# Kernel tuning notes

Measured on AMD Instinct MI355X. Metric: run time of the kernel, lower is better.

## Reference

```python
import jax, jax.numpy as jnp
import numpy as np

NQ = 4096
N0, N1 = 32768, 8192
N = N0 + N1
F = 128          # emb_dim (32x0e+32x1e)
H = 4            # num_heads
HD = F // H
NB = 64          # fc_neurons[0] radial basis size
DEG = 32
CUTOFFS = jnp.array([2.0, 4.0], dtype=jnp.float32)
OFFSETS = jnp.array([0.1, 0.2], dtype=jnp.float32)


def _sph_harm(u):
    # component-normalized real spherical harmonics l=0,1,2 of unit vectors u [E,3]
    x, y, z = u[:, 0], u[:, 1], u[:, 2]
    s3, s15, s5 = 3.0 ** 0.5, 15.0 ** 0.5, 5.0 ** 0.5
    return jnp.stack([
        jnp.ones_like(x),
        s3 * x, s3 * y, s3 * z,
        s15 * x * y, s15 * y * z, 0.5 * s5 * (3.0 * z * z - 1.0),
        s15 * x * z, 0.5 * s15 * (x * x - y * y),
    ], axis=-1)  # [E,9]


def setup_inputs() -> dict:
    key = jax.random.key(0)
    ks = jax.random.split(key, 20)
    E0 = NQ * DEG
    E1 = NQ * DEG
    edge_src = jnp.concatenate([
        jax.random.randint(ks[0], (E0,), 0, N0),
        jax.random.randint(ks[1], (E1,), N0, N),
    ])
    edge_dst = jnp.concatenate([
        jax.random.randint(ks[2], (E0,), 0, NQ),
        jax.random.randint(ks[3], (E1,), 0, NQ),
    ])
    scale_id = jnp.concatenate([jnp.zeros((E0,), jnp.int32), jnp.ones((E1,), jnp.int32)])
    r = lambda k, sh, s=1.0: jax.random.normal(k, sh, jnp.float32) * s
    return {
        'query_coord': r(ks[4], (NQ, 3)),
        'node_feature': r(ks[5], (N, F)),
        'node_coord': r(ks[6], (N, 3)),
        'edge_src': edge_src, 'edge_dst': edge_dst, 'scale_id': scale_id,
        'b_dst': r(ks[7], (F,)),
        'Wq': r(ks[8], (F, F), F ** -0.5),
        'Wk': r(ks[9], (F, F), F ** -0.5),
        'Wv': r(ks[10], (F, F), F ** -0.5),
        'Wo': r(ks[11], (F, F), F ** -0.5),
        'bo': r(ks[12], (F,)),
        'W_rad0': r(ks[13], (NB, NB), NB ** -0.5), 'b_rad0': r(ks[14], (NB,)),
        'W_rad1': r(ks[15], (NB, NB), NB ** -0.5), 'b_rad1': r(ks[16], (NB,)),
        'W_msg': r(ks[17], (NB, F), NB ** -0.5),
        'W_sh': r(ks[18], (9, F), 9 ** -0.5),
        'W_alpha': r(ks[19], (NB, H), NB ** -0.5),
    }


def _forward(query_coord, node_feature, node_coord, b_dst, Wq, Wk, Wv, Wo, bo,
             W_rad0, b_rad0, W_rad1, b_rad1, W_msg, W_sh, W_alpha,
             edge_src, edge_dst, scale_id):
    Nq = query_coord.shape[0]
    vec = node_coord[edge_src] - query_coord[edge_dst]            # [E,3]
    rlen = jnp.sqrt(jnp.sum(vec * vec, -1) + 1e-12)               # [E]
    off = OFFSETS[scale_id]
    cut = CUTOFFS[scale_id]
    xn = (rlen - off) / (cut - off)                               # normalized radius per scale
    centers = jnp.linspace(0.0, 1.0, NB)
    std = 1.0 / NB
    g = jnp.exp(-0.5 * ((xn[:, None] - centers) / std) ** 2)      # [E,NB] gaussian RBF
    soft = 0.5 * (1.0 + jnp.cos(jnp.pi * jnp.clip((xn - 0.8) / 0.2, 0.0, 1.0)))
    g = g * soft[:, None]                                         # soft finite cutoff
    # per-scale Linear after radial basis (2 scales, masked select)
    edge_scalar = jnp.where((scale_id == 0)[:, None], g @ W_rad0 + b_rad0, g @ W_rad1 + b_rad1)
    sh = _sph_harm(vec / rlen[:, None])                           # [E,9]
    # attention GNN (equiformer-style): dst features start as zeros + learned bias
    q = (b_dst @ Wq).reshape(H, HD)
    k = (node_feature @ Wk)[edge_src].reshape(-1, H, HD)
    logits = jnp.einsum('hd,ehd->eh', q, k) / (HD ** 0.5) + edge_scalar @ W_alpha  # [E,H]
    m = jax.ops.segment_max(logits, edge_dst, num_segments=Nq)
    p = jnp.exp(logits - m[edge_dst])
    denom = jax.ops.segment_sum(p, edge_dst, num_segments=Nq)
    alpha = p / (denom[edge_dst] + 1e-9)                          # segment softmax [E,H]
    v_e = (node_feature @ Wv)[edge_src] * (edge_scalar @ W_msg) + sh @ W_sh  # [E,F]
    msg = (alpha[:, :, None] * v_e.reshape(-1, H, HD)).reshape(-1, F)
    out = jax.ops.segment_sum(msg, edge_dst, num_segments=Nq)     # [Nq,F]
    return out @ Wo + bo


def reference(query_coord, node_feature, node_coord, edge_src, edge_dst, scale_id,
              b_dst, Wq, Wk, Wv, Wo, bo, W_rad0, b_rad0, W_rad1, b_rad1,
              W_msg, W_sh, W_alpha):
    return _forward(query_coord, node_feature, node_coord, b_dst, Wq, Wk, Wv, Wo, bo,
                    W_rad0, b_rad0, W_rad1, b_rad1, W_msg, W_sh, W_alpha,
                    edge_src, edge_dst, scale_id)
```

## Files before the change

### kernel.cpp

```cpp
#include <hip/hip_runtime.h>
#include <hip/hip_bf16.h>
#include <math.h>

#define PI_F 3.14159265358979323846f

typedef __attribute__((ext_vector_type(8))) short short8v;
typedef __attribute__((ext_vector_type(4))) float f32x4;

__device__ __forceinline__ short f2bf(float x) {
    return __builtin_bit_cast(short, __float2bfloat16(x));
}
__device__ __forceinline__ float bf2f(unsigned short u) {
    return __uint_as_float(((unsigned)u) << 16);
}
__device__ __forceinline__ int pack_bf2(float a, float b) {
    return (int)(unsigned short)f2bf(a) | ((int)(unsigned short)f2bf(b) << 16);
}

static const size_t WS_WA     = 0;
static const size_t WS_BA     = 512;
static const size_t WS_BM     = 520;
static const size_t WS_WMF    = 776;
static const size_t WS_WSHF   = 8968;
static const size_t WS_QKF    = 11016;
static const size_t WS_WVF    = 12040;
static const size_t WS_WOF    = 20232;
static const size_t WS_COUNTS = 28424;
static const size_t WS_OFFS   = 36624;
static const size_t WS_CURSOR = 44824;
static const size_t WS_PACKED = 53016;
static const size_t WS_LK     = 315160;
static const size_t WS_EDP    = 479000;
static const size_t WS_EDG    = 1527576;
static const size_t WS_VB     = 2576152;
static const size_t WS_OUTPRE = 5197592;

__global__ __launch_bounds__(256) void k_prepfmt(
    const float* b_dst, const float* Wq, const float* Wk,
    const float* W_rad0, const float* b_rad0,
    const float* W_rad1, const float* b_rad1,
    const float* W_msg, const float* W_alpha, const float* Wv,
    const float* Wo, const float* W_sh,
    float* Wa, float* ba, float* bm,
    short* WmF, short* WshF, short* QKF, short* WVF, short* WOF,
    int* counts, int nkey) {
    __shared__ float qs_s[128];
    __shared__ float qk_s[512];
    int t = threadIdx.x;
    int b = blockIdx.x;
    if (b == 0) {
        for (int i = t; i < nkey; i += 256) counts[i] = 0;
        if (t < 128) {
            float acc = 0.f;
            for (int c = 0; c < 128; ++c) acc += b_dst[c] * Wq[c * 128 + t];
            qs_s[t] = acc;
        }
        __syncthreads();
        if (t < 128) {
            const float invs = 0.17677669529663687f;
            for (int h = 0; h < 4; ++h) {
                float acc = 0.f;
                for (int d = 0; d < 32; ++d)
                    acc += Wk[t * 128 + h * 32 + d] * qs_s[h * 32 + d];
                qk_s[t * 4 + h] = acc * invs;
            }
        }
        for (int idx = t; idx < 512; idx += 256) {
            int s = idx >> 8, i = (idx >> 2) & 63, h = idx & 3;
            const float* Wr = s ? W_rad1 : W_rad0;
            float acc = 0.f;
            for (int u = 0; u < 64; ++u) acc += Wr[i * 64 + u] * W_alpha[u * 4 + h];
            Wa[idx] = acc;
        }
        if (t < 8) {
            int s = t >> 2, h = t & 3;
            const float* br = s ? b_rad1 : b_rad0;
            float acc = 0.f;
            for (int u = 0; u < 64; ++u) acc += br[u] * W_alpha[u * 4 + h];
            ba[t] = acc;
        }
        {
            int s = t >> 7, c = t & 127;
            const float* br = s ? b_rad1 : b_rad0;
            float acc = 0.f;
            for (int u = 0; u < 64; ++u) acc += br[u] * W_msg[u * 128 + c];
            bm[t] = acc;
        }
        __syncthreads();
        for (int idx = t; idx < 2048; idx += 256) {
            int j = idx & 7, lane = (idx >> 3) & 63, kh = idx >> 9;
            int k = kh * 32 + ((lane >> 4) << 3) + j;
            int col = lane & 15;
            QKF[idx] = f2bf(col < 4 ? qk_s[k * 4 + col] : 0.f);
        }
    } else {
        int item = (b - 1) * 256 + t;
        if (item < 16384) {
            int j = item & 7, lane = (item >> 3) & 63, kh = (item >> 9) & 1;
            int ct = (item >> 10) & 7, sid = item >> 13;
            int k = kh * 32 + ((lane >> 4) << 3) + j;
            int c = (lane & 15) * 8 + ct;
            const float* Wr = sid ? W_rad1 : W_rad0;
            float acc = 0.f;
            for (int u = 0; u < 64; ++u) acc += Wr[k * 64 + u] * W_msg[u * 128 + c];
            WmF[item] = f2bf(acc);
        } else if (item < 20480) {
            int i2 = item - 16384;
            int j = i2 & 7, lane = (i2 >> 3) & 63, ct = (i2 >> 9) & 7;
            int k = ((lane >> 4) << 3) + j;
            int c = (lane & 15) * 8 + ct;
            WshF[i2] = f2bf(k < 9 ? W_sh[k * 128 + c] : 0.f);
        } else if (item < 36864) {
            int i2 = item - 20480;
            int j = i2 & 7, lane = (i2 >> 3) & 63, ct = (i2 >> 9) & 7, kh = (i2 >> 12) & 3;
            int k = kh * 32 + ((lane >> 4) << 3) + j;
            int c = (lane & 15) * 8 + ct;
            WVF[i2] = f2bf(Wv[k * 128 + c]);
        } else {
            int i2 = item - 36864;
            int j = i2 & 7, lane = (i2 >> 3) & 63, ct = (i2 >> 9) & 7, kh = (i2 >> 12) & 3;
            int k = kh * 32 + ((lane >> 4) << 3) + j;
            int c = (lane & 15) * 8 + ct;
            WOF[i2] = f2bf(Wo[k * 128 + c]);
        }
    }
}

template <typename OUT, bool LK>
__global__ __launch_bounds__(256) void k_mgemm(
    const float* A, const short* WF, const float* bias, OUT* out,
    float* lk, const short* QKF, int M) {
    int t = threadIdx.x;
    int w = t >> 6, lane = t & 63;
    int m = lane & 15, grp = lane >> 4;
    int row0 = (blockIdx.x * 4 + w) * 16;
    if (row0 >= M) return;

    short8v a[4];
#pragma unroll
    for (int kh = 0; kh < 4; ++kh) {
        const float* ap = &A[(size_t)(row0 + m) * 128 + kh * 32 + grp * 8];
        float4 f0 = *(const float4*)ap;
        float4 f1 = *(const float4*)(ap + 4);
        a[kh][0] = f2bf(f0.x); a[kh][1] = f2bf(f0.y);
        a[kh][2] = f2bf(f0.z); a[kh][3] = f2bf(f0.w);
        a[kh][4] = f2bf(f1.x); a[kh][5] = f2bf(f1.y);
        a[kh][6] = f2bf(f1.z); a[kh][7] = f2bf(f1.w);
    }
    if constexpr (LK) {
        f32x4 cl = {0.f, 0.f, 0.f, 0.f};
#pragma unroll
        for (int kh = 0; kh < 4; ++kh) {
            short8v qb = *(const short8v*)&QKF[(kh * 64 + lane) * 8];
            cl = __builtin_amdgcn_mfma_f32_16x16x32_bf16(a[kh], qb, cl, 0, 0, 0);
        }
        if (m < 4) {
#pragma unroll
            for (int r = 0; r < 4; ++r)
                lk[(size_t)(row0 + grp * 4 + r) * 4 + m] = cl[r];
        }
    }
    f32x4 c8[8];
#pragma unroll
    for (int ct = 0; ct < 8; ++ct) {
        f32x4 c = {0.f, 0.f, 0.f, 0.f};
#pragma unroll
        for (int kh = 0; kh < 4; ++kh) {
            short8v bf = *(const short8v*)&WF[((kh * 8 + ct) * 64 + lane) * 8];
            c = __builtin_amdgcn_mfma_f32_16x16x32_bf16(a[kh], bf, c, 0, 0, 0);
        }
        c8[ct] = c;
    }
    if constexpr (sizeof(OUT) == 2) {
#pragma unroll
        for (int r = 0; r < 4; ++r) {
            int row = row0 + grp * 4 + r;
            int4 sv;
            sv.x = pack_bf2(c8[0][r], c8[1][r]);
            sv.y = pack_bf2(c8[2][r], c8[3][r]);
            sv.z = pack_bf2(c8[4][r], c8[5][r]);
            sv.w = pack_bf2(c8[6][r], c8[7][r]);
            *(int4*)&out[(size_t)row * 128 + m * 8] = sv;
        }
    } else {
        float4 b0 = make_float4(0.f, 0.f, 0.f, 0.f), b1 = b0;
        if (bias) {
            b0 = *(const float4*)&bias[m * 8];
            b1 = *(const float4*)&bias[m * 8 + 4];
        }
#pragma unroll
        for (int r = 0; r < 4; ++r) {
            int row = row0 + grp * 4 + r;
            float4 o0 = make_float4(c8[0][r] + b0.x, c8[1][r] + b0.y,
                                    c8[2][r] + b0.z, c8[3][r] + b0.w);
            float4 o1 = make_float4(c8[4][r] + b1.x, c8[5][r] + b1.y,
                                    c8[6][r] + b1.z, c8[7][r] + b1.w);
            *(float4*)&out[(size_t)row * 128 + m * 8] = o0;
            *(float4*)&out[(size_t)row * 128 + m * 8 + 4] = o1;
        }
    }
}

__global__ void k_hist(const int* edge_dst, const int* scale_id, int* counts, int E, int NQr) {
    int e = blockIdx.x * 256 + threadIdx.x;
    if (e < E) atomicAdd(&counts[scale_id[e] * NQr + edge_dst[e]], 1);
}

__global__ void k_scan(const int* counts, int* offsets, int* cursor, int nkey) {
    __shared__ int sdata[256];
    int t = threadIdx.x;
    int chunk = (nkey + 255) / 256;
    int sum = 0;
    for (int i = 0; i < chunk; ++i) {
        int idx = t * chunk + i;
        sum += (idx < nkey) ? counts[idx] : 0;
    }
    sdata[t] = sum;
    __syncthreads();
    for (int off = 1; off < 256; off <<= 1) {
        int v = (t >= off) ? sdata[t - off] : 0;
        __syncthreads();
        sdata[t] += v;
        __syncthreads();
    }
    int run = sdata[t] - sum;
    for (int i = 0; i < chunk; ++i) {
        int idx = t * chunk + i;
        if (idx < nkey) {
            offsets[idx] = run;
            cursor[idx] = run;
            run += counts[idx];
        }
    }
    if (t == 255) offsets[nkey] = sdata[255];
}

__global__ __launch_bounds__(256) void k_scatter_edge(
    const int* edge_src, const int* edge_dst, const int* scale_id,
    const float* qc, const float* nc, const float* lk,
    const float* WaB, const float* baB, int* cursor,
    int* packed, float* edP, float* edG, int E, int NQr) {
    __shared__ float WaS[512];
    __shared__ float baS[8];
    int t = threadIdx.x;
    for (int i = t; i < 512; i += 256) WaS[i] = WaB[i];
    if (t < 8) baS[t] = baB[t];
    __syncthreads();
    int e = blockIdx.x * 256 + t;
    if (e >= E) return;
    int src = edge_src[e], dst = edge_dst[e], sid = scale_id[e];
    int pos = atomicAdd(&cursor[sid * NQr + dst], 1);

    float qx = qc[dst * 3 + 0], qy = qc[dst * 3 + 1], qz = qc[dst * 3 + 2];
    float vx = nc[src * 3 + 0] - qx;
    float vy = nc[src * 3 + 1] - qy;
    float vz = nc[src * 3 + 2] - qz;
    float r = sqrtf(vx * vx + vy * vy + vz * vz + 1e-12f);
    float rinv = 1.0f / r;
    float ux = vx * rinv, uy = vy * rinv, uz = vz * rinv;

    float roff = sid ? 0.2f : 0.1f;
    float rdiv = sid ? (1.0f / 3.8f) : (1.0f / 1.9f);
    float xn = (r - roff) * rdiv;
    float su = fminf(fmaxf((xn - 0.8f) * 5.0f, 0.0f), 1.0f);
    float soft = 0.5f * (1.0f + __cosf(PI_F * su));

    float4 lkv = *(const float4*)&lk[(size_t)src * 4];

    const float qs = 64.f / 63.f;
    const float Qc = __expf(-qs * qs);
    const float* Wrow = WaS + sid * 256;
    float a0 = 0.f, a1 = 0.f, a2 = 0.f, a3 = 0.f;
#pragma unroll
    for (int ch = 0; ch < 8; ++ch) {
        float d = (xn - (float)(ch * 8) * (1.0f / 63.0f)) * 64.0f;
        float g = __expf(-0.5f * d * d);
        float tt = __expf(fminf(qs * d - 0.5f * qs * qs, 60.f));
#pragma unroll
        for (int j = 0; j < 8; ++j) {
            float4 wa = *(const float4*)&Wrow[(ch * 8 + j) * 4];
            a0 = fmaf(g, wa.x, a0);
            a1 = fmaf(g, wa.y, a1);
            a2 = fmaf(g, wa.z, a2);
            a3 = fmaf(g, wa.w, a3);
            g *= tt; tt *= Qc;
        }
    }
    float p0 = __expf(lkv.x + soft * a0 + baS[sid * 4 + 0]);
    float p1 = __expf(lkv.y + soft * a1 + baS[sid * 4 + 1]);
    float p2 = __expf(lkv.z + soft * a2 + baS[sid * 4 + 2]);
    float p3 = __expf(lkv.w + soft * a3 + baS[sid * 4 + 3]);
    packed[pos] = src | (dst << 16);
    *(float4*)&edP[(size_t)pos * 4] = make_float4(p0, p1, p2, p3);
    *(float4*)&edG[(size_t)pos * 4] = make_float4(ux, uy, uz, xn);
}

__device__ __forceinline__ short8v gchain(float xn, int k0, float soft, float Qc) {
    const float qs = 64.f / 63.f;
    float d = (xn - (float)k0 * (1.0f / 63.0f)) * 64.0f;
    float g = __expf(-0.5f * d * d);
    float tt = __expf(fminf(qs * d - 0.5f * qs * qs, 60.f));
    short8v rr;
#pragma unroll
    for (int j = 0; j < 8; ++j) {
        rr[j] = f2bf(g * soft);
        g *= tt; tt *= Qc;
    }
    return rr;
}

__global__ __launch_bounds__(256) void k_main6(
    const int* offsets, const int* packed, const float* edP, const float* edG,
    const unsigned short* Vu, const float* bm, const short* WmF, const short* WshF,
    float* out_pre, int NQr) {
    __shared__ float part[4][136];
    int t = threadIdx.x;
    int w = t >> 6, lane = t & 63;
    int dst = blockIdx.x;
    int sid = w & 1, par = w >> 1;
    int m = lane & 15, grp = lane >> 4;
    int h = m >> 2;

    float acc[8];
#pragma unroll
    for (int i = 0; i < 8; ++i) acc[i] = 0.f;
    float den = 0.f;

    int key = sid * NQr + dst;
    int s0 = offsets[key], s1 = offsets[key + 1];
    int n = s1 - s0;

    float4 bm0 = *(const float4*)&bm[sid * 128 + m * 8];
    float4 bm1 = *(const float4*)&bm[sid * 128 + m * 8 + 4];
    float bmv[8] = {bm0.x, bm0.y, bm0.z, bm0.w, bm1.x, bm1.y, bm1.z, bm1.w};

    const float qs = 64.f / 63.f;
    const float Qc = __expf(-qs * qs);
    const float s3 = 1.7320508075688772f, s15 = 3.872983346207417f, s5 = 2.23606797749979f;

    int ntiles = (n + 15) >> 4;
    if (n > 0 && par < ntiles) {
        auto load_tile = [&](int tl, float4& G4o, float (&pho)[4], int4 (&vvo)[4]) {
            int q0 = s0 + tl * 16;
            int posA = q0 + m; if (posA >= s1) posA = s1 - 1;
            G4o = *(const float4*)&edG[(size_t)posA * 4];
            int srcs[4];
#pragma unroll
            for (int r = 0; r < 4; ++r) {
                int pos = q0 + grp * 4 + r;
                bool valid = pos < s1;
                if (!valid) pos = s1 - 1;
                int wv = packed[pos];
                srcs[r] = wv & 0xFFFF;
                float4 pv = *(const float4*)&edP[(size_t)pos * 4];
                float p = (h & 2) ? ((h & 1) ? pv.w : pv.z)
                                  : ((h & 1) ? pv.y : pv.x);
                pho[r] = valid ? p : 0.f;
            }
#pragma unroll
            for (int r = 0; r < 4; ++r)
                vvo[r] = *(const int4*)&Vu[(size_t)srcs[r] * 128 + m * 8];
        };

        float4 G4c; float phc[4]; int4 vvc[4];
        load_tile(par, G4c, phc, vvc);

        for (int tl = par; tl < ntiles; tl += 2) {
            bool hasNext = (tl + 2) < ntiles;
            float4 G4n; float phn[4]; int4 vvn[4];
            if (hasNext) load_tile(tl + 2, G4n, phn, vvn);

            int wds[4][4] = {{vvc[0].x, vvc[0].y, vvc[0].z, vvc[0].w},
                             {vvc[1].x, vvc[1].y, vvc[1].z, vvc[1].w},
                             {vvc[2].x, vvc[2].y, vvc[2].z, vvc[2].w},
                             {vvc[3].x, vvc[3].y, vvc[3].z, vvc[3].w}};
            den += phc[0] + phc[1] + phc[2] + phc[3];

            float xn = G4c.w;
            float su = fminf(fmaxf((xn - 0.8f) * 5.0f, 0.0f), 1.0f);
            float soft = 0.5f * (1.0f + __cosf(PI_F * su));
            short8v aG0 = gchain(xn, grp * 8, soft, Qc);
            short8v aG1 = gchain(xn, 32 + grp * 8, soft, Qc);

            float ux = G4c.x, uy = G4c.y, uz = G4c.z;
            float sh[9];
            sh[0] = 1.f; sh[1] = s3 * ux; sh[2] = s3 * uy; sh[3] = s3 * uz;
            sh[4] = s15 * ux * uy; sh[5] = s15 * uy * uz;
            sh[6] = 0.5f * s5 * (3.f * uz * uz - 1.f);
            sh[7] = s15 * ux * uz; sh[8] = 0.5f * s15 * (ux * ux - uy * uy);
            short8v aS;
#pragma unroll
            for (int j = 0; j < 8; ++j) {
                float v = (grp == 0) ? sh[j] : ((grp == 1 && j == 0) ? sh[8] : 0.f);
                aS[j] = f2bf(v);
            }

#pragma unroll
            for (int ct = 0; ct < 8; ++ct) {
                short8v b0 = *(const short8v*)&WmF[(((sid * 8 + ct) * 2 + 0) * 64 + lane) * 8];
                short8v b1 = *(const short8v*)&WmF[(((sid * 8 + ct) * 2 + 1) * 64 + lane) * 8];
                short8v bS = *(const short8v*)&WshF[(ct * 64 + lane) * 8];
                f32x4 cms = {0.f, 0.f, 0.f, 0.f};
                cms = __builtin_amdgcn_mfma_f32_16x16x32_bf16(aG0, b0, cms, 0, 0, 0);
                cms = __builtin_amdgcn_mfma_f32_16x16x32_bf16(aG1, b1, cms, 0, 0, 0);
                f32x4 csh = {0.f, 0.f, 0.f, 0.f};
                csh = __builtin_amdgcn_mfma_f32_16x16x32_bf16(aS, bS, csh, 0, 0, 0);
#pragma unroll
                for (int r = 0; r < 4; ++r) {
                    int word = wds[r][ct >> 1];
                    unsigned short vu = (ct & 1) ? (unsigned short)(word >> 16)
                                                 : (unsigned short)(word & 0xFFFF);
                    float vf = bf2f(vu);
                    float ve = fmaf(vf, cms[r] + bmv[ct], csh[r]);
                    acc[ct] = fmaf(phc[r], ve, acc[ct]);
                }
            }

            if (hasNext) {
                G4c = G4n;
#pragma unroll
                for (int r = 0; r < 4; ++r) { phc[r] = phn[r]; vvc[r] = vvn[r]; }
            }
        }
    }

#pragma unroll
    for (int i = 0; i < 8; ++i) {
        acc[i] += __shfl_xor(acc[i], 16);
        acc[i] += __shfl_xor(acc[i], 32);
    }
    den += __shfl_xor(den, 16);
    den += __shfl_xor(den, 32);
    if (lane < 16) {
#pragma unroll
        for (int ct = 0; ct < 8; ++ct) part[w][lane * 8 + ct] = acc[ct];
        if ((lane & 3) == 0) part[w][128 + (lane >> 2)] = den;
    }
    __syncthreads();
    if (t < 128) {
        int hh = t >> 5;
        float s = part[0][t] + part[1][t] + part[2][t] + part[3][t];
        float d = part[0][128 + hh] + part[1][128 + hh] +
                  part[2][128 + hh] + part[3][128 + hh];
        out_pre[(size_t)dst * 128 + t] = s / (d + 1e-9f);
    }
}

extern "C" void kernel_launch(void* const* d_in, const int* in_sizes, int n_in,
                              void* d_out, int out_size, void* d_ws, size_t ws_size,
                              hipStream_t stream) {
    const float* query_coord = (const float*)d_in[0];
    const float* node_feature = (const float*)d_in[1];
    const float* node_coord = (const float*)d_in[2];
    const int* edge_src = (const int*)d_in[3];
    const int* edge_dst = (const int*)d_in[4];
    const int* scale_id = (const int*)d_in[5];
    const float* b_dst = (const float*)d_in[6];
    const float* Wq = (const float*)d_in[7];
    const float* Wk = (const float*)d_in[8];
    const float* Wv = (const float*)d_in[9];
    const float* Wo = (const float*)d_in[10];
    const float* bo = (const float*)d_in[11];
    const float* W_rad0 = (const float*)d_in[12];
    const float* b_rad0 = (const float*)d_in[13];
    const float* W_rad1 = (const float*)d_in[14];
    const float* b_rad1 = (const float*)d_in[15];
    const float* W_msg = (const float*)d_in[16];
    const float* W_sh = (const float*)d_in[17];
    const float* W_alpha = (const float*)d_in[18];
    (void)n_in; (void)ws_size; (void)out_size;

    int NQr = in_sizes[0] / 3;
    int Nn = in_sizes[1] / 128;
    int E = in_sizes[3];
    int nkey = NQr * 2;

    float* ws = (float*)d_ws;
    float* Wa = ws + WS_WA;
    float* ba = ws + WS_BA;
    float* bm = ws + WS_BM;
    short* WmF = (short*)(ws + WS_WMF);
    short* WshF = (short*)(ws + WS_WSHF);
    short* QKF = (short*)(ws + WS_QKF);
    short* WVF = (short*)(ws + WS_WVF);
    short* WOF = (short*)(ws + WS_WOF);
    int* counts = (int*)(ws + WS_COUNTS);
    int* offsets = (int*)(ws + WS_OFFS);
    int* cursor = (int*)(ws + WS_CURSOR);
    int* packed = (int*)(ws + WS_PACKED);
    float* lk = ws + WS_LK;
    float* edP = ws + WS_EDP;
    float* edG = ws + WS_EDG;
    unsigned short* Vb = (unsigned short*)(ws + WS_VB);
    float* out_pre = ws + WS_OUTPRE;
    float* out = (float*)d_out;

    hipLaunchKernelGGL(k_prepfmt, dim3(209), dim3(256), 0, stream,
                       b_dst, Wq, Wk, W_rad0, b_rad0, W_rad1, b_rad1, W_msg, W_alpha,
                       Wv, Wo, W_sh, Wa, ba, bm, WmF, WshF, QKF, WVF, WOF, counts, nkey);
    hipLaunchKernelGGL((k_mgemm<unsigned short, true>), dim3((Nn + 63) / 64), dim3(256), 0,
                       stream, node_feature, WVF, (const float*)nullptr, Vb, lk, QKF, Nn);
    hipLaunchKernelGGL(k_hist, dim3((E + 255) / 256), dim3(256), 0, stream,
                       edge_dst, scale_id, counts, E, NQr);
    hipLaunchKernelGGL(k_scan, dim3(1), dim3(256), 0, stream, counts, offsets, cursor, nkey);
    hipLaunchKernelGGL(k_scatter_edge, dim3((E + 255) / 256), dim3(256), 0, stream,
                       edge_src, edge_dst, scale_id, query_coord, node_coord, lk,
                       Wa, ba, cursor, packed, edP, edG, E, NQr);
    hipLaunchKernelGGL(k_main6, dim3(NQr), dim3(256), 0, stream,
                       offsets, packed, edP, edG, Vb, bm, WmF, WshF, out_pre, NQr);
    hipLaunchKernelGGL((k_mgemm<float, false>), dim3((NQr + 63) / 64), dim3(256), 0, stream,
                       out_pre, WOF, bo, out, (float*)nullptr, (const short*)nullptr, NQr);
}
```

Before: 153.1 us.

## Map one wave per destination in main kernel and fuse histogram into prep

The main aggregation kernel now gives each wavefront a whole destination, walking the tiles of both scales in sequence. Before, four waves per destination split the work by scale and parity and then combined partial sums through shared memory with a block barrier. The edge histogram moves into the prep kernel as extra blocks, and the counts are zeroed with a memset, which removes one launch. The trade-off is less parallelism per destination, so longer serial tile loops per wave and possible load imbalance when degrees vary.

New measurement: 147.0 us. 4.0% less time.

```diff
diff --git a/kernel.cpp b/kernel.cpp
--- a/kernel.cpp
+++ b/kernel.cpp
@@ -41,15 +41,15 @@
     const float* W_rad1, const float* b_rad1,
     const float* W_msg, const float* W_alpha, const float* Wv,
     const float* Wo, const float* W_sh,
+    const int* edge_dst, const int* scale_id,
     float* Wa, float* ba, float* bm,
     short* WmF, short* WshF, short* QKF, short* WVF, short* WOF,
-    int* counts, int nkey) {
+    int* counts, int E, int NQr) {
     __shared__ float qs_s[128];
     __shared__ float qk_s[512];
     int t = threadIdx.x;
     int b = blockIdx.x;
     if (b == 0) {
-        for (int i = t; i < nkey; i += 256) counts[i] = 0;
         if (t < 128) {
             float acc = 0.f;
             for (int c = 0; c < 128; ++c) acc += b_dst[c] * Wq[c * 128 + t];
@@ -93,7 +93,7 @@
             int col = lane & 15;
             QKF[idx] = f2bf(col < 4 ? qk_s[k * 4 + col] : 0.f);
         }
-    } else {
+    } else if (b <= 208) {
         int item = (b - 1) * 256 + t;
         if (item < 16384) {
             int j = item & 7, lane = (item >> 3) & 63, kh = (item >> 9) & 1;
@@ -123,6 +123,9 @@
             int c = (lane & 15) * 8 + ct;
             WOF[i2] = f2bf(Wo[k * 128 + c]);
         }
+    } else {
+        int e = (b - 209) * 256 + t;
+        if (e < E) atomicAdd(&counts[scale_id[e] * NQr + edge_dst[e]], 1);
     }
 }
 
@@ -199,11 +202,6 @@
             *(float4*)&out[(size_t)row * 128 + m * 8 + 4] = o1;
         }
     }
-}
-
-__global__ void k_hist(const int* edge_dst, const int* scale_id, int* counts, int E, int NQr) {
-    int e = blockIdx.x * 256 + threadIdx.x;
-    if (e < E) atomicAdd(&counts[scale_id[e] * NQr + edge_dst[e]], 1);
 }
 
 __global__ void k_scan(const int* counts, int* offsets, int* cursor, int nkey) {
@@ -309,72 +307,82 @@
     return rr;
 }
 
-__global__ __launch_bounds__(256) void k_main6(
+__global__ __launch_bounds__(256) void k_main7(
     const int* offsets, const int* packed, const float* edP, const float* edG,
     const unsigned short* Vu, const float* bm, const short* WmF, const short* WshF,
     float* out_pre, int NQr) {
-    __shared__ float part[4][136];
     int t = threadIdx.x;
     int w = t >> 6, lane = t & 63;
-    int dst = blockIdx.x;
-    int sid = w & 1, par = w >> 1;
+    int dst = blockIdx.x * 4 + w;
+    if (dst >= NQr) return;
     int m = lane & 15, grp = lane >> 4;
     int h = m >> 2;
 
+    int s0a = offsets[dst],       s1a = offsets[dst + 1];
+    int s0b = offsets[NQr + dst], s1b = offsets[NQr + dst + 1];
+    int nt0 = (s1a - s0a + 15) >> 4;
+    int nt1 = (s1b - s0b + 15) >> 4;
+    int ntot = nt0 + nt1;
+
     float acc[8];
 #pragma unroll
     for (int i = 0; i < 8; ++i) acc[i] = 0.f;
     float den = 0.f;
 
-    int key = sid * NQr + dst;
-    int s0 = offsets[key], s1 = offsets[key + 1];
-    int n = s1 - s0;
-
-    float4 bm0 = *(const float4*)&bm[sid * 128 + m * 8];
-    float4 bm1 = *(const float4*)&bm[sid * 128 + m * 8 + 4];
-    float bmv[8] = {bm0.x, bm0.y, bm0.z, bm0.w, bm1.x, bm1.y, bm1.z, bm1.w};
+    float4 bmA0 = *(const float4*)&bm[m * 8];
+    float4 bmA1 = *(const float4*)&bm[m * 8 + 4];
+    float4 bmB0 = *(const float4*)&bm[128 + m * 8];
+    float4 bmB1 = *(const float4*)&bm[128 + m * 8 + 4];
 
     const float qs = 64.f / 63.f;
     const float Qc = __expf(-qs * qs);
     const float s3 = 1.7320508075688772f, s15 = 3.872983346207417f, s5 = 2.23606797749979f;
 
-    int ntiles = (n + 15) >> 4;
-    if (n > 0 && par < ntiles) {
-        auto load_tile = [&](int tl, float4& G4o, float (&pho)[4], int4 (&vvo)[4]) {
-            int q0 = s0 + tl * 16;
-            int posA = q0 + m; if (posA >= s1) posA = s1 - 1;
+    if (ntot > 0) {
+        auto load_tile = [&](int tl, int& sid_o, float4& G4o, float (&pho)[4], int4 (&vvo)[4]) {
+            int sid = (tl >= nt0) ? 1 : 0;
+            int q0  = sid ? (s0b + (tl - nt0) * 16) : (s0a + tl * 16);
+            int lim = sid ? s1b : s1a;
+            int posA = q0 + m; if (posA >= lim) posA = lim - 1;
             G4o = *(const float4*)&edG[(size_t)posA * 4];
             int srcs[4];
 #pragma unroll
             for (int r = 0; r < 4; ++r) {
                 int pos = q0 + grp * 4 + r;
-                bool valid = pos < s1;
-                if (!valid) pos = s1 - 1;
-                int wv = packed[pos];
-                srcs[r] = wv & 0xFFFF;
-                float4 pv = *(const float4*)&edP[(size_t)pos * 4];
-                float p = (h & 2) ? ((h & 1) ? pv.w : pv.z)
-                                  : ((h & 1) ? pv.y : pv.x);
+                bool valid = pos < lim;
+                if (!valid) pos = lim - 1;
+                srcs[r] = packed[pos] & 0xFFFF;
+                float p = edP[(size_t)pos * 4 + h];
                 pho[r] = valid ? p : 0.f;
             }
 #pragma unroll
             for (int r = 0; r < 4; ++r)
                 vvo[r] = *(const int4*)&Vu[(size_t)srcs[r] * 128 + m * 8];
+            sid_o = sid;
         };
 
-        float4 G4c; float phc[4]; int4 vvc[4];
-        load_tile(par, G4c, phc, vvc);
-
-        for (int tl = par; tl < ntiles; tl += 2) {
-            bool hasNext = (tl + 2) < ntiles;
-            float4 G4n; float phn[4]; int4 vvn[4];
-            if (hasNext) load_tile(tl + 2, G4n, phn, vvn);
+        int sidc; float4 G4c; float phc[4]; int4 vvc[4];
+        load_tile(0, sidc, G4c, phc, vvc);
+
+        for (int tl = 0; tl < ntot; ++tl) {
+            bool hasNext = (tl + 1) < ntot;
+            int sidn; float4 G4n; float phn[4]; int4 vvn[4];
+            if (hasNext) load_tile(tl + 1, sidn, G4n, phn, vvn);
 
             int wds[4][4] = {{vvc[0].x, vvc[0].y, vvc[0].z, vvc[0].w},
                              {vvc[1].x, vvc[1].y, vvc[1].z, vvc[1].w},
                              {vvc[2].x, vvc[2].y, vvc[2].z, vvc[2].w},
                              {vvc[3].x, vvc[3].y, vvc[3].z, vvc[3].w}};
             den += phc[0] + phc[1] + phc[2] + phc[3];
+
+            float bmv[8];
+            {
+                float4 b0 = sidc ? bmB0 : bmA0;
+                float4 b1 = sidc ? bmB1 : bmA1;
+                bmv[0] = b0.x; bmv[1] = b0.y; bmv[2] = b0.z; bmv[3] = b0.w;
+                bmv[4] = b1.x; bmv[5] = b1.y; bmv[6] = b1.z; bmv[7] = b1.w;
+            }
+            const short* wmp = WmF + sidc * 8192;
 
             float xn = G4c.w;
             float su = fminf(fmaxf((xn - 0.8f) * 5.0f, 0.0f), 1.0f);
@@ -397,8 +405,8 @@
 
 #pragma unroll
             for (int ct = 0; ct < 8; ++ct) {
-                short8v b0 = *(const short8v*)&WmF[(((sid * 8 + ct) * 2 + 0) * 64 + lane) * 8];
-                short8v b1 = *(const short8v*)&WmF[(((sid * 8 + ct) * 2 + 1) * 64 + lane) * 8];
+                short8v b0 = *(const short8v*)&wmp[((ct * 2 + 0) * 64 + lane) * 8];
+                short8v b1 = *(const short8v*)&wmp[((ct * 2 + 1) * 64 + lane) * 8];
                 short8v bS = *(const short8v*)&WshF[(ct * 64 + lane) * 8];
                 f32x4 cms = {0.f, 0.f, 0.f, 0.f};
                 cms = __builtin_amdgcn_mfma_f32_16x16x32_bf16(aG0, b0, cms, 0, 0, 0);
@@ -417,7 +425,7 @@
             }
 
             if (hasNext) {
-                G4c = G4n;
+                sidc = sidn; G4c = G4n;
 #pragma unroll
                 for (int r = 0; r < 4; ++r) { phc[r] = phn[r]; vvc[r] = vvn[r]; }
             }
@@ -432,17 +440,11 @@
     den += __shfl_xor(den, 16);
     den += __shfl_xor(den, 32);
     if (lane < 16) {
-#pragma unroll
-        for (int ct = 0; ct < 8; ++ct) part[w][lane * 8 + ct] = acc[ct];
-        if ((lane & 3) == 0) part[w][128 + (lane >> 2)] = den;
-    }
-    __syncthreads();
-    if (t < 128) {
-        int hh = t >> 5;
-        float s = part[0][t] + part[1][t] + part[2][t] + part[3][t];
-        float d = part[0][128 + hh] + part[1][128 + hh] +
-                  part[2][128 + hh] + part[3][128 + hh];
-        out_pre[(size_t)dst * 128 + t] = s / (d + 1e-9f);
+        float dinv = 1.0f / (den + 1e-9f);
+        float4 o0 = make_float4(acc[0] * dinv, acc[1] * dinv, acc[2] * dinv, acc[3] * dinv);
+        float4 o1 = make_float4(acc[4] * dinv, acc[5] * dinv, acc[6] * dinv, acc[7] * dinv);
+        *(float4*)&out_pre[(size_t)dst * 128 + m * 8] = o0;
+        *(float4*)&out_pre[(size_t)dst * 128 + m * 8 + 4] = o1;
     }
 }
 
@@ -495,18 +497,19 @@
     float* out_pre = ws + WS_OUTPRE;
     float* out = (float*)d_out;
 
-    hipLaunchKernelGGL(k_prepfmt, dim3(209), dim3(256), 0, stream,
+    hipMemsetAsync(counts, 0, nkey * sizeof(int), stream);
+    int histBlocks = (E + 255) / 256;
+    hipLaunchKernelGGL(k_prepfmt, dim3(209 + histBlocks), dim3(256), 0, stream,
                        b_dst, Wq, Wk, W_rad0, b_rad0, W_rad1, b_rad1, W_msg, W_alpha,
-                       Wv, Wo, W_sh, Wa, ba, bm, WmF, WshF, QKF, WVF, WOF, counts, nkey);
+                       Wv, Wo, W_sh, edge_dst, scale_id,
+                       Wa, ba, bm, WmF, WshF, QKF, WVF, WOF, counts, E, NQr);
     hipLaunchKernelGGL((k_mgemm<unsigned short, true>), dim3((Nn + 63) / 64), dim3(256), 0,
                        stream, node_feature, WVF, (const float*)nullptr, Vb, lk, QKF, Nn);
-    hipLaunchKernelGGL(k_hist, dim3((E + 255) / 256), dim3(256), 0, stream,
-                       edge_dst, scale_id, counts, E, NQr);
     hipLaunchKernelGGL(k_scan, dim3(1), dim3(256), 0, stream, counts, offsets, cursor, nkey);
     hipLaunchKernelGGL(k_scatter_edge, dim3((E + 255) / 256), dim3(256), 0, stream,
                        edge_src, edge_dst, scale_id, query_coord, node_coord, lk,
                        Wa, ba, cursor, packed, edP, edG, E, NQr);
-    hipLaunchKernelGGL(k_main6, dim3(NQr), dim3(256), 0, stream,
+    hipLaunchKernelGGL(k_main7, dim3((NQr + 3) / 4), dim3(256), 0, stream,
                        offsets, packed, edP, edG, Vb, bm, WmF, WshF, out_pre, NQr);
     hipLaunchKernelGGL((k_mgemm<float, false>), dim3((NQr + 63) / 64), dim3(256), 0, stream,
                        out_pre, WOF, bo, out, (float*)nullptr, (const short*)nullptr, NQr);
```
